# Kernel tuning notes

Measured on AMD Instinct MI355X. Metric: run time of the kernel, lower is better.

The kernel has to match this reference:

```python
import jax, jax.numpy as jnp
import numpy as np

EPS = 1e-5

def _bn_relu(z, gamma, beta):
    # BatchNorm1d (training mode: biased batch stats) + ReLU, per-feature over batch dim
    mean = jnp.mean(z, axis=0)
    var = jnp.var(z, axis=0)  # biased, matches torch BN normalization
    zn = (z - mean) * jax.lax.rsqrt(var + EPS) * gamma + beta
    return jax.nn.relu(zn)


def setup_inputs() -> dict:
    key = jax.random.key(0)
    ks = jax.random.split(key, 16)
    N, D_IN, H, D_OUT = 2097152, 16, 32, 1
    def lin(kw, kb, fan_in, fan_out):
        bound = 1.0 / np.sqrt(fan_in)
        W = jax.random.uniform(kw, (fan_out, fan_in), jnp.float32, -bound, bound)
        b = jax.random.uniform(kb, (fan_out,), jnp.float32, -bound, bound)
        return W, b
    W1, b1 = lin(ks[0], ks[1], D_IN, H)
    W2, b2 = lin(ks[2], ks[3], H, H)
    W3, b3 = lin(ks[4], ks[5], H, H)
    W4, b4 = lin(ks[6], ks[7], H, D_OUT)
    x = jax.random.normal(ks[8], (N, D_IN), jnp.float32)
    return {
        "x": x,
        "W1": W1, "b1": b1, "g1": jnp.ones((H,), jnp.float32), "be1": jnp.zeros((H,), jnp.float32),
        "W2": W2, "b2": b2, "g2": jnp.ones((H,), jnp.float32), "be2": jnp.zeros((H,), jnp.float32),
        "W3": W3, "b3": b3, "g3": jnp.ones((H,), jnp.float32), "be3": jnp.zeros((H,), jnp.float32),
        "W4": W4, "b4": b4,
    }


def reference(x, W1, b1, g1, be1, W2, b2, g2, be2, W3, b3, g3, be3, W4, b4):
    p1 = _bn_relu(x @ W1.T + b1, g1, be1)    # [N, H]
    p2 = _bn_relu(p1 @ W2.T + b2, g2, be2)   # [N, H]
    p3 = _bn_relu(p2 @ W3.T + b3, g3, be3)   # [N, H]
    return p3 @ W4.T + b4                    # [N, 1]
```

## Files before the change

### kernel.cpp

```cpp
#include <hip/hip_runtime.h>

#define EPS 1e-5f
#define NTHR 256
#define NBLK 1024
#define NSLOT 16

typedef __bf16 bf16x8 __attribute__((ext_vector_type(8)));
typedef float f32x16 __attribute__((ext_vector_type(16)));


template<int DEPTH>
__global__ __launch_bounds__(NTHR) void k_fwd(
    const float* __restrict__ x, __bf16* __restrict__ xb,
    const float* __restrict__ W1, const float* __restrict__ b1,
    const float* __restrict__ g1, const float* __restrict__ be1,
    const float* __restrict__ W2, const float* __restrict__ b2,
    const float* __restrict__ g2, const float* __restrict__ be2,
    const float* __restrict__ W3, const float* __restrict__ b3,
    const float* __restrict__ g3, const float* __restrict__ be3,
    const float* __restrict__ W4, const float* __restrict__ b4,
    float* __restrict__ stats, float* __restrict__ out, int N)
{
    constexpr bool STATS = (DEPTH < 4);
    __shared__ float s_stat[3][64];
    __shared__ float s_a[3][32];
    __shared__ float s_e[3][32];
    __shared__ float s_w[NTHR / 64][64];

    const int tid = threadIdx.x;
    const float invN = 1.0f / (float)N;

    if (tid < 64) {
        for (int L = 0; L < DEPTH - 1; ++L) {
            float a = 0.f;
            #pragma unroll
            for (int s = 0; s < NSLOT; ++s) a += stats[L * (NSLOT * 64) + s * 64 + tid];
            s_stat[L][tid] = a;
        }
    }
    __syncthreads();
    if (tid < 32) {
        const float* gs[3]  = {g1, g2, g3};
        const float* bes[3] = {be1, be2, be3};
        const float* bs[3]  = {b1, b2, b3};
        for (int L = 0; L < DEPTH - 1; ++L) {
            float mu = s_stat[L][tid] * invN;
            float v  = s_stat[L][32 + tid] * invN - mu * mu;
            float a  = gs[L][tid] * rsqrtf(v + EPS);
            s_a[L][tid] = a;
            s_e[L][tid] = bs[L][tid] - mu + bes[L][tid] / a;
        }
    }
    __syncthreads();

    const int lane = tid & 63;
    const int h = lane >> 5;
    const int ml = lane & 31;

    bf16x8 w1f;
    {
        const float* p = W1 + ml * 16 + h * 8;
        #pragma unroll
        for (int j = 0; j < 8; ++j) w1f[j] = (__bf16)p[j];
    }
    bf16x8 w2f0 = {}, w2f1 = {}, w3f0 = {}, w3f1 = {};
    if (DEPTH >= 2) {
        #pragma unroll
        for (int kh = 0; kh < 2; ++kh)
            #pragma unroll
            for (int j = 0; j < 8; ++j) {
                int pk = (j & 3) + 8 * (j >> 2) + 4 * h + 16 * kh;
                float v = W2[ml * 32 + pk] * s_a[0][pk];
                if (kh == 0) w2f0[j] = (__bf16)v; else w2f1[j] = (__bf16)v;
            }
    }
    if (DEPTH >= 3) {
        #pragma unroll
        for (int kh = 0; kh < 2; ++kh)
            #pragma unroll
            for (int j = 0; j < 8; ++j) {
                int pk = (j & 3) + 8 * (j >> 2) + 4 * h + 16 * kh;
                float v = W3[ml * 32 + pk] * s_a[1][pk];
                if (kh == 0) w3f0[j] = (__bf16)v; else w3f1[j] = (__bf16)v;
            }
    }

    f32x16 c1, c2 = {}, c3 = {};
    float w4c[16];
    #pragma unroll
    for (int i = 0; i < 16; ++i) {
        int p = (i & 3) + 8 * (i >> 2) + 4 * h;
        c1[i] = (DEPTH == 1) ? b1[p] : s_e[0][p];
        if (DEPTH >= 2) c2[i] = (DEPTH == 2) ? b2[p] : s_e[1][p];
        if (DEPTH >= 3) c3[i] = (DEPTH == 3) ? b3[p] : s_e[2][p];
        if (DEPTH == 4) w4c[i] = W4[p] * s_a[2][p]; else w4c[i] = 0.f;
    }
    const float b4v = (DEPTH == 4) ? b4[0] : 0.f;

    const int ntiles = N >> 5;
    const int nwaves = NBLK * (NTHR / 64);
    const int gwave  = blockIdx.x * (NTHR / 64) + (tid >> 6);
    const int tpw    = ntiles / nwaves;
    const int rem    = ntiles - tpw * nwaves;
    const int t0     = gwave * tpw + (gwave < rem ? gwave : rem);
    const int cnt    = tpw + (gwave < rem ? 1 : 0);

    float sums[16], sqs[16];
    #pragma unroll
    for (int i = 0; i < 16; ++i) { sums[i] = 0.f; sqs[i] = 0.f; }

    auto tile = [&](int t, bf16x8 xf) {
        f32x16 a1 = __builtin_amdgcn_mfma_f32_32x32x16_bf16(w1f, xf, c1, 0, 0, 0);
        if (DEPTH == 1) {
            #pragma unroll
            for (int i = 0; i < 16; ++i) { sums[i] += a1[i]; sqs[i] = fmaf(a1[i], a1[i], sqs[i]); }
            return;
        }
        bf16x8 qa, qb;
        #pragma unroll
        for (int j = 0; j < 8; ++j) {
            qa[j] = (__bf16)fmaxf(a1[j], 0.f);
            qb[j] = (__bf16)fmaxf(a1[8 + j], 0.f);
        }
        f32x16 a2 = __builtin_amdgcn_mfma_f32_32x32x16_bf16(w2f0, qa, c2, 0, 0, 0);
        a2 = __builtin_amdgcn_mfma_f32_32x32x16_bf16(w2f1, qb, a2, 0, 0, 0);
        if (DEPTH == 2) {
            #pragma unroll
            for (int i = 0; i < 16; ++i) { sums[i] += a2[i]; sqs[i] = fmaf(a2[i], a2[i], sqs[i]); }
            return;
        }
        bf16x8 pa, pb;
        #pragma unroll
        for (int j = 0; j < 8; ++j) {
            pa[j] = (__bf16)fmaxf(a2[j], 0.f);
            pb[j] = (__bf16)fmaxf(a2[8 + j], 0.f);
        }
        f32x16 a3 = __builtin_amdgcn_mfma_f32_32x32x16_bf16(w3f0, pa, c3, 0, 0, 0);
        a3 = __builtin_amdgcn_mfma_f32_32x32x16_bf16(w3f1, pb, a3, 0, 0, 0);
        if (DEPTH == 3) {
            #pragma unroll
            for (int i = 0; i < 16; ++i) { sums[i] += a3[i]; sqs[i] = fmaf(a3[i], a3[i], sqs[i]); }
            return;
        }
        float o = 0.f;
        #pragma unroll
        for (int i = 0; i < 16; ++i) o = fmaf(w4c[i], fmaxf(a3[i], 0.f), o);
        o += __shfl_xor(o, 32);
        if (h == 0) out[(t << 5) + ml] = o + b4v;
    };

    auto cvt = [&](float4 a, float4 b) -> bf16x8 {
        bf16x8 xf;
        xf[0] = (__bf16)a.x; xf[1] = (__bf16)a.y; xf[2] = (__bf16)a.z; xf[3] = (__bf16)a.w;
        xf[4] = (__bf16)b.x; xf[5] = (__bf16)b.y; xf[6] = (__bf16)b.z; xf[7] = (__bf16)b.w;
        return xf;
    };

    const int nb4 = cnt & ~3;
    if (DEPTH == 1) {
        for (int i0 = 0; i0 < nb4; i0 += 4) {
            const float* base = x + (size_t)((t0 + i0) << 5) * 16;
            const float4* p0 = (const float4*)(base + (size_t)(ml)      * 16 + h * 8);
            const float4* p1 = (const float4*)(base + (size_t)(32 + ml) * 16 + h * 8);
            const float4* p2 = (const float4*)(base + (size_t)(64 + ml) * 16 + h * 8);
            const float4* p3 = (const float4*)(base + (size_t)(96 + ml) * 16 + h * 8);
            float4 a0 = p0[0], b0 = p0[1];
            float4 a1 = p1[0], b1_ = p1[1];
            float4 a2 = p2[0], b2_ = p2[1];
            float4 a3 = p3[0], b3_ = p3[1];
            bf16x8 x0 = cvt(a0, b0), x1 = cvt(a1, b1_), x2 = cvt(a2, b2_), x3 = cvt(a3, b3_);
            __bf16* w = xb + ((size_t)(t0 + i0) * 64 + lane) * 8;
            *(bf16x8*)(w)        = x0;
            *(bf16x8*)(w + 512)  = x1;
            *(bf16x8*)(w + 1024) = x2;
            *(bf16x8*)(w + 1536) = x3;
            tile(t0 + i0,     x0);
            tile(t0 + i0 + 1, x1);
            tile(t0 + i0 + 2, x2);
            tile(t0 + i0 + 3, x3);
        }
        for (int i = nb4; i < cnt; ++i) {
            int row = ((t0 + i) << 5) + ml;
            const float4* xp = (const float4*)(x + (size_t)row * 16 + h * 8);
            bf16x8 xf = cvt(xp[0], xp[1]);
            *(bf16x8*)(xb + ((size_t)(t0 + i) * 64 + lane) * 8) = xf;
            tile(t0 + i, xf);
        }
    } else {
        for (int i0 = 0; i0 < nb4; i0 += 4) {
            const __bf16* r = xb + ((size_t)(t0 + i0) * 64 + lane) * 8;
            bf16x8 x0 = *(const bf16x8*)(r);
            bf16x8 x1 = *(const bf16x8*)(r + 512);
            bf16x8 x2 = *(const bf16x8*)(r + 1024);
            bf16x8 x3 = *(const bf16x8*)(r + 1536);
            tile(t0 + i0,     x0);
            tile(t0 + i0 + 1, x1);
            tile(t0 + i0 + 2, x2);
            tile(t0 + i0 + 3, x3);
        }
        for (int i = nb4; i < cnt; ++i) {
            bf16x8 xf = *(const bf16x8*)(xb + ((size_t)(t0 + i) * 64 + lane) * 8);
            tile(t0 + i, xf);
        }
    }

    if (STATS) {
        const int wid = tid >> 6;
        #pragma unroll
        for (int i = 0; i < 16; ++i) {
            float s = sums[i], q = sqs[i];
            #pragma unroll
            for (int d = 1; d <= 16; d <<= 1) {
                s += __shfl_xor(s, d);
                q += __shfl_xor(q, d);
            }
            if (ml == 0) {
                int p = (i & 3) + 8 * (i >> 2) + 4 * h;
                s_w[wid][p] = s;
                s_w[wid][32 + p] = q;
            }
        }
        __syncthreads();
        if (tid < 64) {
            float a = s_w[0][tid] + s_w[1][tid] + s_w[2][tid] + s_w[3][tid];
            int L = DEPTH - 1;
            atomicAdd(&stats[L * (NSLOT * 64) + (blockIdx.x & (NSLOT - 1)) * 64 + tid], a);
        }
    }
}

extern "C" void kernel_launch(void* const* d_in, const int* in_sizes, int n_in,
                              void* d_out, int out_size, void* d_ws, size_t ws_size,
                              hipStream_t stream) {
    const float* x   = (const float*)d_in[0];
    const float* W1  = (const float*)d_in[1];
    const float* b1  = (const float*)d_in[2];
    const float* g1  = (const float*)d_in[3];
    const float* be1 = (const float*)d_in[4];
    const float* W2  = (const float*)d_in[5];
    const float* b2  = (const float*)d_in[6];
    const float* g2  = (const float*)d_in[7];
    const float* be2 = (const float*)d_in[8];
    const float* W3  = (const float*)d_in[9];
    const float* b3  = (const float*)d_in[10];
    const float* g3  = (const float*)d_in[11];
    const float* be3 = (const float*)d_in[12];
    const float* W4  = (const float*)d_in[13];
    const float* b4  = (const float*)d_in[14];
    float* out = (float*)d_out;
    int N = in_sizes[0] / 16;

    __bf16* xb   = (__bf16*)d_ws;
    float* stats = (float*)((char*)d_ws + (size_t)N * 16 * 2);

    hipMemsetAsync(stats, 0, 3 * NSLOT * 64 * sizeof(float), stream);

    k_fwd<1><<<NBLK, NTHR, 0, stream>>>(x, xb, W1, b1, g1, be1, W2, b2, g2, be2, W3, b3, g3, be3, W4, b4, stats, out, N);
    k_fwd<2><<<NBLK, NTHR, 0, stream>>>(x, xb, W1, b1, g1, be1, W2, b2, g2, be2, W3, b3, g3, be3, W4, b4, stats, out, N);
    k_fwd<3><<<NBLK, NTHR, 0, stream>>>(x, xb, W1, b1, g1, be1, W2, b2, g2, be2, W3, b3, g3, be3, W4, b4, stats, out, N);
    k_fwd<4><<<NBLK, NTHR, 0, stream>>>(x, xb, W1, b1, g1, be1, W2, b2, g2, be2, W3, b3, g3, be3, W4, b4, stats, out, N);
}
```

Baseline: 314.9 us.

## Double the grid, prefetch x loads in layer one, batch eight bf16 tile reads

Doubles the block count. In the first pass, the next group of four fp32 x tiles is loaded before the current group is computed, which software-pipelines global loads against MFMA work. Later passes load eight cached bf16 tiles at a time instead of four, so more memory requests are in flight. Register pressure rises and may cut occupancy, and more blocks means more partial-statistics reduction work.

```diff
diff --git a/kernel.cpp b/kernel.cpp
--- a/kernel.cpp
+++ b/kernel.cpp
@@ -2,7 +2,7 @@
 
 #define EPS 1e-5f
 #define NTHR 256
-#define NBLK 1024
+#define NBLK 2048
 #define NSLOT 16
 
 typedef __bf16 bf16x8 __attribute__((ext_vector_type(8)));
@@ -31,6 +31,7 @@
     const float invN = 1.0f / (float)N;
 
     if (tid < 64) {
+        #pragma unroll
         for (int L = 0; L < DEPTH - 1; ++L) {
             float a = 0.f;
             #pragma unroll
@@ -43,6 +44,7 @@
         const float* gs[3]  = {g1, g2, g3};
         const float* bes[3] = {be1, be2, be3};
         const float* bs[3]  = {b1, b2, b3};
+        #pragma unroll
         for (int L = 0; L < DEPTH - 1; ++L) {
             float mu = s_stat[L][tid] * invN;
             float v  = s_stat[L][32 + tid] * invN - mu * mu;
@@ -156,51 +158,64 @@
         return xf;
     };
 
-    const int nb4 = cnt & ~3;
     if (DEPTH == 1) {
-        for (int i0 = 0; i0 < nb4; i0 += 4) {
-            const float* base = x + (size_t)((t0 + i0) << 5) * 16;
-            const float4* p0 = (const float4*)(base + (size_t)(ml)      * 16 + h * 8);
-            const float4* p1 = (const float4*)(base + (size_t)(32 + ml) * 16 + h * 8);
-            const float4* p2 = (const float4*)(base + (size_t)(64 + ml) * 16 + h * 8);
-            const float4* p3 = (const float4*)(base + (size_t)(96 + ml) * 16 + h * 8);
-            float4 a0 = p0[0], b0 = p0[1];
-            float4 a1 = p1[0], b1_ = p1[1];
-            float4 a2 = p2[0], b2_ = p2[1];
-            float4 a3 = p3[0], b3_ = p3[1];
-            bf16x8 x0 = cvt(a0, b0), x1 = cvt(a1, b1_), x2 = cvt(a2, b2_), x3 = cvt(a3, b3_);
+        const int nb4 = cnt & ~3;
+        float4 ua[4], ub[4];
+        auto load4 = [&](int i0, float4* a, float4* b) {
+            #pragma unroll
+            for (int k = 0; k < 4; ++k) {
+                const float4* p = (const float4*)(x + (size_t)((((t0 + i0 + k)) << 5) + ml) * 16 + h * 8);
+                a[k] = p[0]; b[k] = p[1];
+            }
+        };
+        auto comp4 = [&](int i0, const float4* a, const float4* b) {
+            bf16x8 xf[4];
+            #pragma unroll
+            for (int k = 0; k < 4; ++k) xf[k] = cvt(a[k], b[k]);
             __bf16* w = xb + ((size_t)(t0 + i0) * 64 + lane) * 8;
-            *(bf16x8*)(w)        = x0;
-            *(bf16x8*)(w + 512)  = x1;
-            *(bf16x8*)(w + 1024) = x2;
-            *(bf16x8*)(w + 1536) = x3;
-            tile(t0 + i0,     x0);
-            tile(t0 + i0 + 1, x1);
-            tile(t0 + i0 + 2, x2);
-            tile(t0 + i0 + 3, x3);
-        }
-        for (int i = nb4; i < cnt; ++i) {
-            int row = ((t0 + i) << 5) + ml;
-            const float4* xp = (const float4*)(x + (size_t)row * 16 + h * 8);
-            bf16x8 xf = cvt(xp[0], xp[1]);
-            *(bf16x8*)(xb + ((size_t)(t0 + i) * 64 + lane) * 8) = xf;
-            tile(t0 + i, xf);
+            #pragma unroll
+            for (int k = 0; k < 4; ++k) *(bf16x8*)(w + k * 512) = xf[k];
+            #pragma unroll
+            for (int k = 0; k < 4; ++k) tile(t0 + i0 + k, xf[k]);
+        };
+        int i0 = 0;
+        if (nb4) load4(0, ua, ub);
+        for (; i0 + 4 < nb4; i0 += 4) {
+            float4 va[4], vb[4];
+            load4(i0 + 4, va, vb);
+            comp4(i0, ua, ub);
+            #pragma unroll
+            for (int k = 0; k < 4; ++k) { ua[k] = va[k]; ub[k] = vb[k]; }
+        }
+        if (nb4) { comp4(i0, ua, ub); i0 = nb4; }
+        for (; i0 < cnt; ++i0) {
+            const float4* p = (const float4*)(x + (size_t)(((t0 + i0) << 5) + ml) * 16 + h * 8);
+            bf16x8 xf = cvt(p[0], p[1]);
+            *(bf16x8*)(xb + ((size_t)(t0 + i0) * 64 + lane) * 8) = xf;
+            tile(t0 + i0, xf);
         }
     } else {
-        for (int i0 = 0; i0 < nb4; i0 += 4) {
+        const int nb8 = cnt & ~7;
+        int i0 = 0;
+        for (; i0 < nb8; i0 += 8) {
             const __bf16* r = xb + ((size_t)(t0 + i0) * 64 + lane) * 8;
-            bf16x8 x0 = *(const bf16x8*)(r);
-            bf16x8 x1 = *(const bf16x8*)(r + 512);
-            bf16x8 x2 = *(const bf16x8*)(r + 1024);
-            bf16x8 x3 = *(const bf16x8*)(r + 1536);
-            tile(t0 + i0,     x0);
-            tile(t0 + i0 + 1, x1);
-            tile(t0 + i0 + 2, x2);
-            tile(t0 + i0 + 3, x3);
-        }
-        for (int i = nb4; i < cnt; ++i) {
-            bf16x8 xf = *(const bf16x8*)(xb + ((size_t)(t0 + i) * 64 + lane) * 8);
-            tile(t0 + i, xf);
+            bf16x8 v[8];
+            #pragma unroll
+            for (int k = 0; k < 8; ++k) v[k] = *(const bf16x8*)(r + (size_t)k * 512);
+            #pragma unroll
+            for (int k = 0; k < 8; ++k) tile(t0 + i0 + k, v[k]);
+        }
+        for (; i0 + 4 <= cnt; i0 += 4) {
+            const __bf16* r = xb + ((size_t)(t0 + i0) * 64 + lane) * 8;
+            bf16x8 v[4];
+            #pragma unroll
+            for (int k = 0; k < 4; ++k) v[k] = *(const bf16x8*)(r + (size_t)k * 512);
+            #pragma unroll
+            for (int k = 0; k < 4; ++k) tile(t0 + i0 + k, v[k]);
+        }
+        for (; i0 < cnt; ++i0) {
+            bf16x8 xf = *(const bf16x8*)(xb + ((size_t)(t0 + i0) * 64 + lane) * 8);
+            tile(t0 + i0, xf);
         }
     }
 
```

New measurement: 367.0 us. 16.5% more time.
